# Optimization experiments

Hardware: AMD Instinct MI355X
Metric: run time of the kernel (lower is better)

The kernel has to match this reference:

```python
import jax, jax.numpy as jnp
import numpy as np
from jax.scipy.special import gammainc

HUBREG_ITERS = 2
LAYERS = 3


def huber_psi(x, c):
    # Huber influence function: identity inside [-c, c], clipped outside.
    return jnp.where(jnp.abs(x) <= c, x, c * jnp.sign(x))


def chi2_cdf(x, df):
    return gammainc(df / 2.0, x / 2.0)


def hubreg_batched(beta, D, Y, mask, c, lamda, mu, sigma0):
    """Batched Huber regression with IRLS-style scale update.

    beta: [q, r]  one coefficient vector per regression (columns of Y)
    D:    [p, r]  shared design rows; regression j uses rows where mask[:, j] == 1
    Y:    [p, q]  targets, zero where unobserved
    mask: [p, q]  observation indicator (float)
    """
    p, r = D.shape
    cd = jax.lax.stop_gradient(c)  # original detaches c for alpha
    alpha = 0.5 * cd**2 * (1.0 - chi2_cdf(cd**2, 1.0)) + 0.5 * chi2_cdf(cd**2, 3.0)
    P = (D[:, :, None] * D[:, None, :]).reshape(p, r * r)  # [p, r^2]
    G = (mask.T @ P).reshape(-1, r, r)                     # [q, r, r]
    Ginv = jnp.linalg.inv(G)
    nobs = mask.sum(axis=0)                                # [q]
    sigma = sigma0 * jnp.ones((Y.shape[1],), Y.dtype)
    for _ in range(HUBREG_ITERS):
        R = (Y - D @ beta.T) * mask                        # masked residuals [p, q]
        psi = huber_psi(R / sigma[None, :], c)             # zero where mask is zero
        tau = jnp.sqrt((psi * psi).sum(axis=0)) / jnp.sqrt(2.0 * nobs * alpha)
        sigma = sigma * tau**lamda
        psi2 = huber_psi(R / sigma[None, :], c)
        rhs = D.T @ (psi2 * sigma[None, :])                # [r, q] = D[rows].T @ (psi*sigma)
        delta = jnp.einsum('qij,jq->qi', Ginv, rhs)
        beta = beta + mu * delta
    return beta


def setup_inputs() -> dict:
    key = jax.random.key(0)
    k1, k2, k3, k4 = jax.random.split(key, 4)
    m, n, r = 4096, 4096, 10
    U = jax.random.normal(k1, (m, r), jnp.float32)
    V = jax.random.normal(k2, (r, n), jnp.float32)
    obs = (jax.random.uniform(k3, (m, n)) < 0.5).astype(jnp.float32)
    X = jax.random.normal(k4, (m, n), jnp.float32) * obs  # zeros = missing entries
    return {
        "U": U, "V": V, "X": X,
        "c": jnp.float32(1.345), "lamda": jnp.float32(1.0),
        "mu": jnp.float32(0.5), "sigma": jnp.float32(1.0),
    }


def reference(U, V, X, c, lamda, mu, sigma):
    mask = (X != 0).astype(X.dtype)
    for _ in range(LAYERS):
        V = hubreg_batched(V.T, U, X, mask, c, lamda, mu, sigma).T
        U = hubreg_batched(U, V.T, X.T, mask.T, c, lamda, mu, sigma)
    return U @ V
```

## Files before the change

kernel.cpp:

```cpp
#include <hip/hip_runtime.h>
#include <math.h>

#define RNK 10
#define NG  55
#define TPB 256
#define TPBU 64
#define GJ   64
#define GWRD 4
#define GROWS_B (4 * GWRD * 32)
#define GSUBP (GWRD * 32 * 12 + 8)
#define ROWS_P 64
#define ITILE 16

typedef float f2 __attribute__((ext_vector_type(2)));

__device__ __forceinline__ constexpr int tri(int a, int b) { return a*(a+1)/2 + b; }
constexpr int BASE2[10] = {0,0,1,2,4,6,9,12,16,20};

__device__ __forceinline__ float qsum(float v) {
    v += __shfl_xor(v, 1);
    v += __shfl_xor(v, 2);
    return v;
}

__global__ void init_kernel(const float* __restrict__ Uin, const float* __restrict__ Vin,
                            const float* __restrict__ cptr,
                            float* __restrict__ Ut, float* __restrict__ Vc,
                            float* __restrict__ Urow, float* __restrict__ Vrow,
                            float* __restrict__ Gbuf, float* __restrict__ tauacc,
                            float* __restrict__ rhs, float* __restrict__ alpha,
                            int m, int n, int qmax) {
    int idx = blockIdx.x * TPB + threadIdx.x;
    if (idx == 0) {
        float c  = *cptr;
        float A  = erff(c * 0.70710678118654752f);
        float B  = c * 0.79788456080286536f * expf(-0.5f*c*c);
        *alpha = 0.5f*c*c*(1.0f - A) + 0.5f*(A - B);
    }
    if (idx < RNK * m) { int k = idx / m, i = idx - k*m; Ut[idx] = Uin[i*RNK + k]; }
    if (idx < RNK * m) Urow[idx] = Uin[idx];
    if (idx < RNK * n) Vc[idx] = Vin[idx];
    if (idx < RNK * n) { int j = idx / RNK, k = idx - j*RNK; Vrow[idx] = Vin[k*n + j]; }
    if (idx < (NG + 1) * qmax) Gbuf[idx] = 0.0f;
    if (idx < qmax) tauacc[idx] = 0.0f;
    if (idx < RNK * qmax) rhs[idx] = 0.0f;
}

__global__ void transpose_kernel(const float* __restrict__ X, float* __restrict__ XT,
                                 unsigned* __restrict__ maskV, unsigned* __restrict__ maskU,
                                 int m, int n) {
    __shared__ float tile[32][33];
    int bx = blockIdx.x * 32, by = blockIdx.y * 32;
    int tx = threadIdx.x, ty = threadIdx.y;
    #pragma unroll
    for (int dy = 0; dy < 32; dy += 8)
        tile[ty+dy][tx] = X[(size_t)(by+ty+dy)*n + bx + tx];
    __syncthreads();
    #pragma unroll
    for (int dy = 0; dy < 32; dy += 8)
        XT[(size_t)(bx+ty+dy)*m + by + tx] = tile[tx][ty+dy];
    if (ty == 0) {
        unsigned wv = 0;
        #pragma unroll
        for (int u = 0; u < 32; ++u)
            wv |= (tile[u][tx] != 0.0f ? 1u : 0u) << u;
        maskV[(size_t)blockIdx.y * n + bx + tx] = wv;
    } else if (ty == 1) {
        unsigned wu = 0;
        #pragma unroll
        for (int u = 0; u < 32; ++u)
            wu |= (tile[tx][u] != 0.0f ? 1u : 0u) << u;
        maskU[(size_t)blockIdx.x * m + by + tx] = wu;
    }
}

__global__ __launch_bounds__(TPB)
void gram_kernel(const unsigned* __restrict__ mask, const float* __restrict__ Drow,
                 float* __restrict__ Gbuf, int q, int p) {
    __shared__ __align__(16) float Dld[4 * GSUBP];
    int lane = threadIdx.x & 63, wave = threadIdx.x >> 6;
    int jo = lane >> 2, sub = lane & 3;
    int j  = blockIdx.x * GJ + wave * 16 + jo;
    int ib = blockIdx.y * GROWS_B;
    for (int t = threadIdx.x; t < GROWS_B * RNK; t += TPB) {
        int row = t / RNK, k = t - row * RNK;
        Dld[(row >> 7) * GSUBP + (row & 127) * 12 + k] = Drow[(size_t)ib * RNK + t];
    }
    __syncthreads();
    f2 acc2[25];
    float accs[5];
    #pragma unroll
    for (int k = 0; k < 25; ++k) acc2[k] = (f2){0.0f, 0.0f};
    #pragma unroll
    for (int k = 0; k < 5; ++k) accs[k] = 0.0f;
    unsigned cnt = 0;
    int w0 = blockIdx.y * (4 * GWRD) + sub * GWRD;
    const float* dbase = Dld + sub * GSUBP;
    unsigned wnext = mask[(size_t)w0 * q + j];
    for (int wi = 0; wi < GWRD; ++wi) {
        unsigned word = wnext;
        int wn = (wi + 1 < GWRD) ? (wi + 1) : (GWRD - 1);
        wnext = mask[(size_t)(w0 + wn) * q + j];
        cnt += __popc(word);
        const float* drow = dbase + wi * (32 * 12);
        #pragma unroll
        for (int u = 0; u < 32; ++u) {
            float f = (float)((word >> u) & 1u);
            f2 d2[5];
            #pragma unroll
            for (int k = 0; k < 5; ++k) d2[k] = *(const f2*)(drow + u * 12 + 2 * k);
            #pragma unroll
            for (int a = 0; a < RNK; ++a) {
                float da = d2[a >> 1][a & 1];
                float t  = f * da;
                f2 tv = {t, t};
                #pragma unroll
                for (int pb = 0; pb < (a + 1) / 2; ++pb)
                    acc2[BASE2[a] + pb] =
                        __builtin_elementwise_fma(tv, d2[pb], acc2[BASE2[a] + pb]);
                if ((a & 1) == 0) accs[a >> 1] = fmaf(t, da, accs[a >> 1]);
            }
        }
    }
    #pragma unroll
    for (int k = 0; k < 25; ++k) {
        acc2[k][0] = qsum(acc2[k][0]);
        acc2[k][1] = qsum(acc2[k][1]);
    }
    #pragma unroll
    for (int k = 0; k < 5; ++k) accs[k] = qsum(accs[k]);
    float fc = qsum((float)cnt);
    if (sub == 0) {
        #pragma unroll
        for (int a = 0; a < RNK; ++a) {
            #pragma unroll
            for (int pb = 0; pb < (a + 1) / 2; ++pb) {
                atomicAdd(&Gbuf[tri(a, 2*pb)   * q + j], acc2[BASE2[a] + pb][0]);
                atomicAdd(&Gbuf[tri(a, 2*pb+1) * q + j], acc2[BASE2[a] + pb][1]);
            }
            if ((a & 1) == 0) atomicAdd(&Gbuf[tri(a, a) * q + j], accs[a >> 1]);
        }
        atomicAdd(&Gbuf[NG * q + j], fc);
    }
}

__global__ __launch_bounds__(TPB)
void pass1_kernel(const float* __restrict__ Y, const float* __restrict__ Drow,
                  const float* __restrict__ Bm, const float* __restrict__ sigstore,
                  const float* __restrict__ sigma0p, const float* __restrict__ cptr,
                  float* __restrict__ tauacc, int q, int p, int use_store) {
    __shared__ __align__(16) float Dp[ROWS_P][12];
    int j  = blockIdx.x * TPB + threadIdx.x;
    int i0 = blockIdx.y * ROWS_P;
    for (int t = threadIdx.x; t < ROWS_P * RNK; t += TPB) {
        int row = t / RNK, k = t - row * RNK;
        Dp[row][k] = Drow[(size_t)i0 * RNK + t];
    }
    __syncthreads();
    f2 b2[5];
    #pragma unroll
    for (int k = 0; k < 5; ++k)
        b2[k] = (f2){Bm[(2*k)*q + j], Bm[(2*k+1)*q + j]};
    float csg = (*cptr) * (use_store ? sigstore[j] : *sigma0p);
    float a0 = 0.0f;
    float y[8];
    #pragma unroll
    for (int u = 0; u < 8; ++u) y[u] = Y[(size_t)(i0+u)*q + j];
    for (int g = 0; g < ROWS_P; g += 8) {
        float yn[8];
        if (g + 8 < ROWS_P) {
            #pragma unroll
            for (int u = 0; u < 8; ++u) yn[u] = Y[(size_t)(i0+g+8+u)*q + j];
        } else {
            #pragma unroll
            for (int u = 0; u < 8; ++u) yn[u] = 0.0f;
        }
        #pragma unroll
        for (int u = 0; u < 8; ++u) {
            int rl = g + u;
            f2 dot2 = {0.0f, 0.0f};
            #pragma unroll
            for (int k = 0; k < 5; ++k) {
                f2 d2 = *(const f2*)&Dp[rl][2*k];
                dot2 = __builtin_elementwise_fma(d2, b2[k], dot2);
            }
            float dot = dot2[0] + dot2[1];
            float r = (y[u] != 0.0f) ? y[u] - dot : 0.0f;
            r = fminf(fmaxf(r, -csg), csg);
            a0 = fmaf(r, r, a0);
        }
        #pragma unroll
        for (int u = 0; u < 8; ++u) y[u] = yn[u];
    }
    atomicAdd(&tauacc[j], a0);
}

__global__ __launch_bounds__(TPB)
void pass2_kernel(const float* __restrict__ Y, const float* __restrict__ Drow,
                  const float* __restrict__ Bm, const float* __restrict__ Gbuf,
                  const float* __restrict__ tauacc, float* __restrict__ sigstore,
                  const float* __restrict__ cptr, const float* __restrict__ alphap,
                  const float* __restrict__ lamdap, const float* __restrict__ sigma0p,
                  float* __restrict__ rhs, int q, int p, int mode) {
    __shared__ __align__(16) float Dp[ROWS_P][12];
    int j  = blockIdx.x * TPB + threadIdx.x;
    int i0 = blockIdx.y * ROWS_P;
    for (int t = threadIdx.x; t < ROWS_P * RNK; t += TPB) {
        int row = t / RNK, k = t - row * RNK;
        Dp[row][k] = Drow[(size_t)i0 * RNK + t];
    }
    __syncthreads();
    f2 b2[5];
    #pragma unroll
    for (int k = 0; k < 5; ++k)
        b2[k] = (f2){Bm[(2*k)*q + j], Bm[(2*k+1)*q + j]};
    float so  = mode ? sigstore[j] : *sigma0p;
    float nb  = Gbuf[NG*q + j];
    float tau = sqrtf(tauacc[j] / (2.0f * nb * (*alphap))) / so;
    float sg  = so * powf(tau, *lamdap);
    if (mode == 0 && blockIdx.y == 0) sigstore[j] = sg;
    float csg = (*cptr) * sg;

    f2 a2[5];
    #pragma unroll
    for (int k = 0; k < 5; ++k) a2[k] = (f2){0.0f, 0.0f};
    float y[8];
    #pragma unroll
    for (int u = 0; u < 8; ++u) y[u] = Y[(size_t)(i0+u)*q + j];
    for (int g = 0; g < ROWS_P; g += 8) {
        float yn[8];
        if (g + 8 < ROWS_P) {
            #pragma unroll
            for (int u = 0; u < 8; ++u) yn[u] = Y[(size_t)(i0+g+8+u)*q + j];
        } else {
            #pragma unroll
            for (int u = 0; u < 8; ++u) yn[u] = 0.0f;
        }
        #pragma unroll
        for (int u = 0; u < 8; ++u) {
            int rl = g + u;
            f2 d2[5];
            #pragma unroll
            for (int k = 0; k < 5; ++k) d2[k] = *(const f2*)&Dp[rl][2*k];
            f2 dot2 = {0.0f, 0.0f};
            #pragma unroll
            for (int k = 0; k < 5; ++k)
                dot2 = __builtin_elementwise_fma(d2[k], b2[k], dot2);
            float dot = dot2[0] + dot2[1];
            float r = (y[u] != 0.0f) ? y[u] - dot : 0.0f;
            r = fminf(fmaxf(r, -csg), csg);
            f2 rv = {r, r};
            #pragma unroll
            for (int k = 0; k < 5; ++k)
                a2[k] = __builtin_elementwise_fma(d2[k], rv, a2[k]);
        }
        #pragma unroll
        for (int u = 0; u < 8; ++u) y[u] = yn[u];
    }
    #pragma unroll
    for (int k = 0; k < 5; ++k) {
        atomicAdd(&rhs[(2*k)*q   + j], a2[k][0]);
        atomicAdd(&rhs[(2*k+1)*q + j], a2[k][1]);
    }
}

__global__ __launch_bounds__(TPBU)
void update_kernel(float* __restrict__ Gbuf, float* __restrict__ rhs,
                   float* __restrict__ Bm, float* __restrict__ Brow,
                   const float* __restrict__ mup,
                   float* __restrict__ tauacc, int q, int zero_g) {
    int j = blockIdx.x * TPBU + threadIdx.x;
    if (j >= q) return;
    float g[NG];
    #pragma unroll
    for (int k = 0; k < NG; ++k) g[k] = Gbuf[k*q + j];
    #pragma unroll
    for (int a = 0; a < RNK; ++a) {
        #pragma unroll
        for (int b = 0; b < a; ++b) {
            float s = g[tri(a,b)];
            #pragma unroll
            for (int k = 0; k < b; ++k) s -= g[tri(a,k)] * g[tri(b,k)];
            g[tri(a,b)] = s / g[tri(b,b)];
        }
        float s = g[tri(a,a)];
        #pragma unroll
        for (int k = 0; k < a; ++k) s -= g[tri(a,k)] * g[tri(a,k)];
        g[tri(a,a)] = sqrtf(s);
    }
    float x[RNK];
    #pragma unroll
    for (int k = 0; k < RNK; ++k) x[k] = rhs[k*q + j];
    #pragma unroll
    for (int a = 0; a < RNK; ++a) {
        float s = x[a];
        #pragma unroll
        for (int k = 0; k < a; ++k) s -= g[tri(a,k)] * x[k];
        x[a] = s / g[tri(a,a)];
    }
    #pragma unroll
    for (int a = RNK-1; a >= 0; --a) {
        float s = x[a];
        #pragma unroll
        for (int k = a+1; k < RNK; ++k) s -= g[tri(k,a)] * x[k];
        x[a] = s / g[tri(a,a)];
    }
    float mu = *mup;
    #pragma unroll
    for (int k = 0; k < RNK; ++k) {
        float nb = Bm[k*q + j] + mu * x[k];
        Bm[k*q + j] = nb;
        Brow[(size_t)j*RNK + k] = nb;
    }
    tauacc[j] = 0.0f;
    #pragma unroll
    for (int k = 0; k < RNK; ++k) rhs[k*q + j] = 0.0f;
    if (zero_g) {
        #pragma unroll
        for (int k = 0; k <= NG; ++k) Gbuf[k*q + j] = 0.0f;
    }
}

__global__ void gemm_kernel(const float* __restrict__ Ut, const float* __restrict__ Vc,
                            float* __restrict__ out, int m, int n) {
    int j  = blockIdx.x * TPB + threadIdx.x;
    int i0 = blockIdx.y * ITILE;
    float v[RNK];
    #pragma unroll
    for (int k = 0; k < RNK; ++k) v[k] = Vc[k*n + j];
    for (int i = i0; i < i0 + ITILE; ++i) {
        float acc = 0.0f;
        #pragma unroll
        for (int k = 0; k < RNK; ++k) acc = fmaf(Ut[k*m + i], v[k], acc);
        out[(size_t)i*n + j] = acc;
    }
}


namespace {
struct Scratch {
    float *Ut, *Vc, *Urow, *Vrow, *Gbuf, *rhs, *sigma, *tauacc, *alpha;
    unsigned *maskV, *maskU;
};

static void hubreg(const float* Y, const unsigned* mask, const float* Drow,
                   float* Bm, float* Brow, int q, int p,
                   const float* c, const float* lamda, const float* mu, const float* sigma0,
                   const Scratch& s, hipStream_t stream) {
    dim3 gg(q / GJ, p / GROWS_B);
    dim3 gp(q / TPB, p / ROWS_P);
    dim3 gj(q / TPBU);

    gram_kernel  <<<gg, TPB, 0, stream>>>(mask, Drow, s.Gbuf, q, p);
    pass1_kernel <<<gp, TPB, 0, stream>>>(Y, Drow, Bm, s.sigma, sigma0, c, s.tauacc, q, p, 0);
    pass2_kernel <<<gp, TPB, 0, stream>>>(Y, Drow, Bm, s.Gbuf, s.tauacc, s.sigma, c,
                                          s.alpha, lamda, sigma0, s.rhs, q, p, 0);
    update_kernel<<<gj, TPBU, 0, stream>>>(s.Gbuf, s.rhs, Bm, Brow, mu, s.tauacc, q, 0);
    pass1_kernel <<<gp, TPB, 0, stream>>>(Y, Drow, Bm, s.sigma, sigma0, c, s.tauacc, q, p, 1);
    pass2_kernel <<<gp, TPB, 0, stream>>>(Y, Drow, Bm, s.Gbuf, s.tauacc, s.sigma, c,
                                          s.alpha, lamda, sigma0, s.rhs, q, p, 1);
    update_kernel<<<gj, TPBU, 0, stream>>>(s.Gbuf, s.rhs, Bm, Brow, mu, s.tauacc, q, 1);
}
}

extern "C" void kernel_launch(void* const* d_in, const int* in_sizes, int n_in,
                              void* d_out, int out_size, void* d_ws, size_t ws_size,
                              hipStream_t stream) {
    const float* Uin    = (const float*)d_in[0];
    const float* Vin    = (const float*)d_in[1];
    const float* X      = (const float*)d_in[2];
    const float* c      = (const float*)d_in[3];
    const float* lamda  = (const float*)d_in[4];
    const float* mu     = (const float*)d_in[5];
    const float* sigma0 = (const float*)d_in[6];
    float* out = (float*)d_out;

    const int m = in_sizes[0] / RNK;
    const int n = in_sizes[1] / RNK;
    const int qmax = (m > n) ? m : n;

    float* w = (float*)d_ws;
    auto align64 = [](size_t x) { return (x + 63) & ~(size_t)63; };
    size_t off = 0;
    Scratch s;
    s.Ut     = w + off; off = align64(off + (size_t)RNK * m);
    s.Vc     = w + off; off = align64(off + (size_t)RNK * n);
    s.Urow   = w + off; off = align64(off + (size_t)RNK * m);
    s.Vrow   = w + off; off = align64(off + (size_t)RNK * n);
    s.Gbuf   = w + off; off = align64(off + (size_t)(NG + 1) * qmax);
    s.rhs    = w + off; off = align64(off + (size_t)RNK * qmax);
    s.sigma  = w + off; off = align64(off + (size_t)qmax);
    s.tauacc = w + off; off = align64(off + (size_t)qmax);
    s.alpha  = w + off; off = align64(off + 64);
    s.maskV  = (unsigned*)(w + off); off = align64(off + (size_t)(m/32) * n);
    s.maskU  = (unsigned*)(w + off); off = align64(off + (size_t)(n/32) * m);
    (void)ws_size; (void)n_in; (void)out_size;

    {
        int tot = (NG + 1) * qmax;
        init_kernel<<<(tot + TPB - 1) / TPB, TPB, 0, stream>>>(
            Uin, Vin, c, s.Ut, s.Vc, s.Urow, s.Vrow, s.Gbuf, s.tauacc, s.rhs,
            s.alpha, m, n, qmax);
    }
    transpose_kernel<<<dim3(n / 32, m / 32), dim3(32, 8), 0, stream>>>(
        X, out, s.maskV, s.maskU, m, n);

    for (int layer = 0; layer < 3; ++layer) {
        hubreg(X,   s.maskV, s.Urow, s.Vc, s.Vrow, n, m, c, lamda, mu, sigma0, s, stream);
        hubreg(out, s.maskU, s.Vrow, s.Ut, s.Urow, m, n, c, lamda, mu, sigma0, s, stream);
    }

    gemm_kernel<<<dim3(n / TPB, m / ITILE), TPB, 0, stream>>>(s.Ut, s.Vc, out, m, n);
}
```

Measured before the change: 850.2 us.

## Replace Gram atomics with per-block partial buffers and double row-load batch

The Gram kernel now writes its per-row-block partial sums to a dedicated partial buffer instead of issuing 55 atomicAdds per column. The update kernel then reduces over the partitions itself, and only the count slot still needs zeroing. Separately, the pass1/pass2 kernels prefetch Y in batches of 16 rows instead of 8, giving more loads in flight at the cost of more registers. The partial buffer adds workspace and adds sequential reads in the update kernel, whose launch has few threads.

Result: slower. 901.3 us (+6.0%).

```diff
diff --git a/kernel.cpp b/kernel.cpp
--- a/kernel.cpp
+++ b/kernel.cpp
@@ -76,7 +76,7 @@
 
 __global__ __launch_bounds__(TPB)
 void gram_kernel(const unsigned* __restrict__ mask, const float* __restrict__ Drow,
-                 float* __restrict__ Gbuf, int q, int p) {
+                 float* __restrict__ Gpart, float* __restrict__ Gbuf, int q, int p) {
     __shared__ __align__(16) float Dld[4 * GSUBP];
     int lane = threadIdx.x & 63, wave = threadIdx.x >> 6;
     int jo = lane >> 2, sub = lane & 3;
@@ -131,14 +131,15 @@
     for (int k = 0; k < 5; ++k) accs[k] = qsum(accs[k]);
     float fc = qsum((float)cnt);
     if (sub == 0) {
+        float* gp = Gpart + (size_t)blockIdx.y * NG * q + j;
         #pragma unroll
         for (int a = 0; a < RNK; ++a) {
             #pragma unroll
             for (int pb = 0; pb < (a + 1) / 2; ++pb) {
-                atomicAdd(&Gbuf[tri(a, 2*pb)   * q + j], acc2[BASE2[a] + pb][0]);
-                atomicAdd(&Gbuf[tri(a, 2*pb+1) * q + j], acc2[BASE2[a] + pb][1]);
+                gp[(size_t)tri(a, 2*pb)   * q] = acc2[BASE2[a] + pb][0];
+                gp[(size_t)tri(a, 2*pb+1) * q] = acc2[BASE2[a] + pb][1];
             }
-            if ((a & 1) == 0) atomicAdd(&Gbuf[tri(a, a) * q + j], accs[a >> 1]);
+            if ((a & 1) == 0) gp[(size_t)tri(a, a) * q] = accs[a >> 1];
         }
         atomicAdd(&Gbuf[NG * q + j], fc);
     }
@@ -163,20 +164,20 @@
         b2[k] = (f2){Bm[(2*k)*q + j], Bm[(2*k+1)*q + j]};
     float csg = (*cptr) * (use_store ? sigstore[j] : *sigma0p);
     float a0 = 0.0f;
-    float y[8];
-    #pragma unroll
-    for (int u = 0; u < 8; ++u) y[u] = Y[(size_t)(i0+u)*q + j];
-    for (int g = 0; g < ROWS_P; g += 8) {
-        float yn[8];
-        if (g + 8 < ROWS_P) {
-            #pragma unroll
-            for (int u = 0; u < 8; ++u) yn[u] = Y[(size_t)(i0+g+8+u)*q + j];
+    float y[16];
+    #pragma unroll
+    for (int u = 0; u < 16; ++u) y[u] = Y[(size_t)(i0+u)*q + j];
+    for (int g = 0; g < ROWS_P; g += 16) {
+        float yn[16];
+        if (g + 16 < ROWS_P) {
+            #pragma unroll
+            for (int u = 0; u < 16; ++u) yn[u] = Y[(size_t)(i0+g+16+u)*q + j];
         } else {
             #pragma unroll
-            for (int u = 0; u < 8; ++u) yn[u] = 0.0f;
-        }
-        #pragma unroll
-        for (int u = 0; u < 8; ++u) {
+            for (int u = 0; u < 16; ++u) yn[u] = 0.0f;
+        }
+        #pragma unroll
+        for (int u = 0; u < 16; ++u) {
             int rl = g + u;
             f2 dot2 = {0.0f, 0.0f};
             #pragma unroll
@@ -190,7 +191,7 @@
             a0 = fmaf(r, r, a0);
         }
         #pragma unroll
-        for (int u = 0; u < 8; ++u) y[u] = yn[u];
+        for (int u = 0; u < 16; ++u) y[u] = yn[u];
     }
     atomicAdd(&tauacc[j], a0);
 }
@@ -224,20 +225,20 @@
     f2 a2[5];
     #pragma unroll
     for (int k = 0; k < 5; ++k) a2[k] = (f2){0.0f, 0.0f};
-    float y[8];
-    #pragma unroll
-    for (int u = 0; u < 8; ++u) y[u] = Y[(size_t)(i0+u)*q + j];
-    for (int g = 0; g < ROWS_P; g += 8) {
-        float yn[8];
-        if (g + 8 < ROWS_P) {
-            #pragma unroll
-            for (int u = 0; u < 8; ++u) yn[u] = Y[(size_t)(i0+g+8+u)*q + j];
+    float y[16];
+    #pragma unroll
+    for (int u = 0; u < 16; ++u) y[u] = Y[(size_t)(i0+u)*q + j];
+    for (int g = 0; g < ROWS_P; g += 16) {
+        float yn[16];
+        if (g + 16 < ROWS_P) {
+            #pragma unroll
+            for (int u = 0; u < 16; ++u) yn[u] = Y[(size_t)(i0+g+16+u)*q + j];
         } else {
             #pragma unroll
-            for (int u = 0; u < 8; ++u) yn[u] = 0.0f;
-        }
-        #pragma unroll
-        for (int u = 0; u < 8; ++u) {
+            for (int u = 0; u < 16; ++u) yn[u] = 0.0f;
+        }
+        #pragma unroll
+        for (int u = 0; u < 16; ++u) {
             int rl = g + u;
             f2 d2[5];
             #pragma unroll
@@ -255,7 +256,7 @@
                 a2[k] = __builtin_elementwise_fma(d2[k], rv, a2[k]);
         }
         #pragma unroll
-        for (int u = 0; u < 8; ++u) y[u] = yn[u];
+        for (int u = 0; u < 16; ++u) y[u] = yn[u];
     }
     #pragma unroll
     for (int k = 0; k < 5; ++k) {
@@ -265,15 +266,21 @@
 }
 
 __global__ __launch_bounds__(TPBU)
-void update_kernel(float* __restrict__ Gbuf, float* __restrict__ rhs,
+void update_kernel(const float* __restrict__ Gpart, float* __restrict__ Gbuf,
+                   float* __restrict__ rhs,
                    float* __restrict__ Bm, float* __restrict__ Brow,
                    const float* __restrict__ mup,
-                   float* __restrict__ tauacc, int q, int zero_g) {
+                   float* __restrict__ tauacc, int q, int npart, int zero_g) {
     int j = blockIdx.x * TPBU + threadIdx.x;
     if (j >= q) return;
     float g[NG];
     #pragma unroll
-    for (int k = 0; k < NG; ++k) g[k] = Gbuf[k*q + j];
+    for (int k = 0; k < NG; ++k) g[k] = Gpart[(size_t)k * q + j];
+    for (int y = 1; y < npart; ++y) {
+        const float* gp = Gpart + (size_t)y * NG * q + j;
+        #pragma unroll
+        for (int k = 0; k < NG; ++k) g[k] += gp[(size_t)k * q];
+    }
     #pragma unroll
     for (int a = 0; a < RNK; ++a) {
         #pragma unroll
@@ -315,10 +322,7 @@
     tauacc[j] = 0.0f;
     #pragma unroll
     for (int k = 0; k < RNK; ++k) rhs[k*q + j] = 0.0f;
-    if (zero_g) {
-        #pragma unroll
-        for (int k = 0; k <= NG; ++k) Gbuf[k*q + j] = 0.0f;
-    }
+    if (zero_g) Gbuf[NG*q + j] = 0.0f;
 }
 
 __global__ void gemm_kernel(const float* __restrict__ Ut, const float* __restrict__ Vc,
@@ -339,7 +343,7 @@
 
 namespace {
 struct Scratch {
-    float *Ut, *Vc, *Urow, *Vrow, *Gbuf, *rhs, *sigma, *tauacc, *alpha;
+    float *Ut, *Vc, *Urow, *Vrow, *Gbuf, *Gpart, *rhs, *sigma, *tauacc, *alpha;
     unsigned *maskV, *maskU;
 };
 
@@ -347,19 +351,22 @@
                    float* Bm, float* Brow, int q, int p,
                    const float* c, const float* lamda, const float* mu, const float* sigma0,
                    const Scratch& s, hipStream_t stream) {
-    dim3 gg(q / GJ, p / GROWS_B);
+    int npart = p / GROWS_B;
+    dim3 gg(q / GJ, npart);
     dim3 gp(q / TPB, p / ROWS_P);
     dim3 gj(q / TPBU);
 
-    gram_kernel  <<<gg, TPB, 0, stream>>>(mask, Drow, s.Gbuf, q, p);
+    gram_kernel  <<<gg, TPB, 0, stream>>>(mask, Drow, s.Gpart, s.Gbuf, q, p);
     pass1_kernel <<<gp, TPB, 0, stream>>>(Y, Drow, Bm, s.sigma, sigma0, c, s.tauacc, q, p, 0);
     pass2_kernel <<<gp, TPB, 0, stream>>>(Y, Drow, Bm, s.Gbuf, s.tauacc, s.sigma, c,
                                           s.alpha, lamda, sigma0, s.rhs, q, p, 0);
-    update_kernel<<<gj, TPBU, 0, stream>>>(s.Gbuf, s.rhs, Bm, Brow, mu, s.tauacc, q, 0);
+    update_kernel<<<gj, TPBU, 0, stream>>>(s.Gpart, s.Gbuf, s.rhs, Bm, Brow, mu,
+                                           s.tauacc, q, npart, 0);
     pass1_kernel <<<gp, TPB, 0, stream>>>(Y, Drow, Bm, s.sigma, sigma0, c, s.tauacc, q, p, 1);
     pass2_kernel <<<gp, TPB, 0, stream>>>(Y, Drow, Bm, s.Gbuf, s.tauacc, s.sigma, c,
                                           s.alpha, lamda, sigma0, s.rhs, q, p, 1);
-    update_kernel<<<gj, TPBU, 0, stream>>>(s.Gbuf, s.rhs, Bm, Brow, mu, s.tauacc, q, 1);
+    update_kernel<<<gj, TPBU, 0, stream>>>(s.Gpart, s.Gbuf, s.rhs, Bm, Brow, mu,
+                                           s.tauacc, q, npart, 1);
 }
 }
 
@@ -378,6 +385,7 @@
     const int m = in_sizes[0] / RNK;
     const int n = in_sizes[1] / RNK;
     const int qmax = (m > n) ? m : n;
+    const int npmax = qmax / GROWS_B;
 
     float* w = (float*)d_ws;
     auto align64 = [](size_t x) { return (x + 63) & ~(size_t)63; };
@@ -388,6 +396,7 @@
     s.Urow   = w + off; off = align64(off + (size_t)RNK * m);
     s.Vrow   = w + off; off = align64(off + (size_t)RNK * n);
     s.Gbuf   = w + off; off = align64(off + (size_t)(NG + 1) * qmax);
+    s.Gpart  = w + off; off = align64(off + (size_t)npmax * NG * qmax);
     s.rhs    = w + off; off = align64(off + (size_t)RNK * qmax);
     s.sigma  = w + off; off = align64(off + (size_t)qmax);
     s.tauacc = w + off; off = align64(off + (size_t)qmax);
```
